# Performance work log

Hardware: AMD Instinct MI355X
Metric: run time of the kernel (lower is better)

The kernel has to match this reference:

```python
import jax, jax.numpy as jnp
from jax import lax
import numpy as np

N_HEADS, N_FEATURES, IMG_W, IMG_H, C_DOWN = 8, 64, 96, 96, 32


def setup_inputs() -> dict:
    key = jax.random.key(0)
    ks = jax.random.split(key, 16)
    d = {
        'X': jax.random.normal(ks[0], (N_FEATURES, IMG_W, IMG_H), jnp.float32),
        'WQ_task': jax.random.normal(ks[1], (N_HEADS, N_FEATURES, 1, 1), jnp.float32),
        'BQ_task': jax.random.normal(ks[2], (N_HEADS, N_FEATURES, 1, 1), jnp.float32),
        'WK_task': jax.random.normal(ks[3], (N_FEATURES, 1, 1), jnp.float32),
        'BK_task': jax.random.normal(ks[4], (N_FEATURES, 1, 1), jnp.float32),
        'WV_task': jax.random.normal(ks[5], (1, C_DOWN, 1, 1), jnp.float32),
        'BV_task': jax.random.normal(ks[6], (1, C_DOWN, 1, 1), jnp.float32),
        # learned parameters (loaded from disk in the original)
        'WQ_t_minus_1': jax.random.uniform(ks[7], (N_HEADS, N_FEATURES, 1, 1), jnp.float32),
        'WQ_x': jax.random.uniform(ks[8], (1, N_FEATURES, 1, 1), jnp.float32),
        'BQ': jax.random.uniform(ks[9], (N_HEADS, N_FEATURES, 1, 1), jnp.float32),
        'WK_x': jax.random.uniform(ks[10], (N_FEATURES, 1, 1), jnp.float32),
        'BK': jax.random.uniform(ks[11], (N_FEATURES, 1, 1), jnp.float32),
        'Vconv_w': jax.random.normal(ks[12], (C_DOWN, N_FEATURES, 3, 3), jnp.float32) * 0.05,
        'Vconv_b': jax.random.normal(ks[13], (C_DOWN,), jnp.float32) * 0.05,
        # recurrent state (zeros at t=0 in original; random here to exercise the path)
        'prev_Q': jax.random.normal(ks[14], (N_HEADS, N_FEATURES, IMG_W, IMG_H), jnp.float32),
    }
    return d


def reference(X, WQ_task, BQ_task, WK_task, BK_task, WV_task, BV_task,
              WQ_t_minus_1, WQ_x, BQ, WK_x, BK, Vconv_w, Vconv_b, prev_Q):
    F, W, H = X.shape
    rx = X[None]  # (1, F, W, H)
    # Q: (A, F, W, H);  K: (F, W, H)
    Q = WQ_task * jax.nn.relu(WQ_t_minus_1 * prev_Q + WQ_x * rx + BQ) + BQ_task
    K = WK_task * jax.nn.relu(WK_x * X + BK) + BK_task
    # similarity[w,h,u,v] = sum_{a,f} Q[a,f,w,h] * K[f,u,v]
    #                     = sum_f (sum_a Q)[f,w,h] * K[f,u,v]  -> a (WH,F)@(F,WH) GEMM
    Qs = Q.sum(axis=0)  # (F, W, H)
    sim = jnp.einsum('fwh,fuv->whuv', Qs, K)  # (W, H, W, H)
    attn = jax.nn.softmax(sim.reshape(W, H, W * H), axis=-1)  # (W, H, WH)
    # V = task-modulated 3x3 conv of X
    Vc = lax.conv_general_dilated(rx, Vconv_w, window_strides=(1, 1), padding='SAME',
                                  dimension_numbers=('NCHW', 'OIHW', 'NCHW'))
    Vc = Vc + Vconv_b[None, :, None, None]
    V = (WV_task * Vc + BV_task)[0].reshape(C_DOWN, W * H)  # (C, WH)
    # out[c,w,h] = sum_k attn[w,h,k] * V[c,k]
    out = jnp.einsum('whk,ck->cwh', attn, V)  # (C, W, H)
    return out
```

## Files before the change

### kernel.cpp

```cpp
#include <hip/hip_runtime.h>

#define WH 9216
#define NF 64
#define NC 32
#define NH 8
#define IMGW 96
#define IMGH 96
#define PW 98
#define PPLANE 9604
#define L2E 1.4426950408889634f
#define DEFER 11.5f

typedef float f32x4 __attribute__((ext_vector_type(4)));
typedef short short8 __attribute__((ext_vector_type(8)));

__device__ inline short bf16_bits(float x) {
  __bf16 h = (__bf16)x;
  return __builtin_bit_cast(short, h);
}
__device__ inline float bf16_round(float x) { return (float)(__bf16)x; }

__global__ __launch_bounds__(256, 2) void prep_kernel(
    const float* __restrict__ X, const float* __restrict__ WQ_task,
    const float* __restrict__ BQ_task, const float* __restrict__ WK_task,
    const float* __restrict__ BK_task, const float* __restrict__ WQ_t1,
    const float* __restrict__ WQ_x, const float* __restrict__ BQ,
    const float* __restrict__ WK_x, const float* __restrict__ BK,
    const float* __restrict__ prevQ, const float* __restrict__ Wc,
    const float* __restrict__ WV_task,
    short* __restrict__ qfrag, short* __restrict__ kfrag,
    unsigned short* __restrict__ padXT, short8* __restrict__ wfrag)
{
  const int bid = blockIdx.x;
  const int t = threadIdx.x;
  if (bid < 576) {
    const int lane = t & 63;
    const int w2 = t >> 6;
    const int fh = w2 & 1, sub = w2 >> 1;
    const int h = lane >> 4;
    const int T = bid;
    const int wh = T * 16 + (lane & 15);
    const int f0 = fh * 32 + 8 * h + 4 * sub;

    float x[4];
    #pragma unroll
    for (int e = 0; e < 4; ++e) x[e] = X[(size_t)(f0 + e) * WH + wh];
    float pq[32];
    #pragma unroll
    for (int a = 0; a < NH; ++a)
      #pragma unroll
      for (int e = 0; e < 4; ++e)
        pq[a * 4 + e] = prevQ[(size_t)(a * 64 + f0 + e) * WH + wh];

    const float4 wkx = *(const float4*)&WK_x[f0];
    const float4 bk  = *(const float4*)&BK[f0];
    const float4 wkt = *(const float4*)&WK_task[f0];
    const float4 bkt = *(const float4*)&BK_task[f0];
    const float4 wqx = *(const float4*)&WQ_x[f0];

    float q[4], k[4], xq[4];
    k[0] = fmaf(wkt.x, fmaxf(fmaf(wkx.x, x[0], bk.x), 0.f), bkt.x);
    k[1] = fmaf(wkt.y, fmaxf(fmaf(wkx.y, x[1], bk.y), 0.f), bkt.y);
    k[2] = fmaf(wkt.z, fmaxf(fmaf(wkx.z, x[2], bk.z), 0.f), bkt.z);
    k[3] = fmaf(wkt.w, fmaxf(fmaf(wkx.w, x[3], bk.w), 0.f), bkt.w);
    xq[0] = wqx.x * x[0]; xq[1] = wqx.y * x[1];
    xq[2] = wqx.z * x[2]; xq[3] = wqx.w * x[3];
    q[0] = q[1] = q[2] = q[3] = 0.f;
    #pragma unroll
    for (int a = 0; a < NH; ++a) {
      const int af0 = a * 64 + f0;
      const float4 w1  = *(const float4*)&WQ_t1[af0];
      const float4 bq  = *(const float4*)&BQ[af0];
      const float4 wqt = *(const float4*)&WQ_task[af0];
      const float4 bqt = *(const float4*)&BQ_task[af0];
      q[0] = fmaf(wqt.x, fmaxf(fmaf(w1.x, pq[a * 4 + 0], xq[0] + bq.x), 0.f), q[0]) + bqt.x;
      q[1] = fmaf(wqt.y, fmaxf(fmaf(w1.y, pq[a * 4 + 1], xq[1] + bq.y), 0.f), q[1]) + bqt.y;
      q[2] = fmaf(wqt.z, fmaxf(fmaf(w1.z, pq[a * 4 + 2], xq[2] + bq.z), 0.f), q[2]) + bqt.z;
      q[3] = fmaf(wqt.w, fmaxf(fmaf(w1.w, pq[a * 4 + 3], xq[3] + bq.w), 0.f), q[3]) + bqt.w;
    }

    short4 qh, ql, kh, klo;
    {
      float qs0 = q[0] * L2E, qs1 = q[1] * L2E, qs2 = q[2] * L2E, qs3 = q[3] * L2E;
      qh.x = bf16_bits(qs0); ql.x = bf16_bits(qs0 - bf16_round(qs0));
      qh.y = bf16_bits(qs1); ql.y = bf16_bits(qs1 - bf16_round(qs1));
      qh.z = bf16_bits(qs2); ql.z = bf16_bits(qs2 - bf16_round(qs2));
      qh.w = bf16_bits(qs3); ql.w = bf16_bits(qs3 - bf16_round(qs3));
      kh.x = bf16_bits(k[0]); klo.x = bf16_bits(k[0] - bf16_round(k[0]));
      kh.y = bf16_bits(k[1]); klo.y = bf16_bits(k[1] - bf16_round(k[1]));
      kh.z = bf16_bits(k[2]); klo.z = bf16_bits(k[2] - bf16_round(k[2]));
      kh.w = bf16_bits(k[3]); klo.w = bf16_bits(k[3] - bf16_round(k[3]));
    }
    const size_t offh = ((size_t)(T * 4 + fh) * 64 + lane) * 8 + sub * 4;
    const size_t offl = ((size_t)(T * 4 + 2 + fh) * 64 + lane) * 8 + sub * 4;
    *(short4*)&qfrag[offh] = qh;
    *(short4*)&qfrag[offl] = ql;
    *(short4*)&kfrag[offh] = kh;
    *(short4*)&kfrag[offl] = klo;
  } else if (bid < 877) {
    const int idx = (bid - 576) * 256 + t;
    if (idx < 76832) {
      const int fi = idx / PPLANE;
      const int p = idx - fi * PPLANE;
      const int pw = p / PW;
      const int ph = p - pw * PW;
      short8 r;
      if (pw >= 1 && pw <= IMGW && ph >= 1 && ph <= IMGH) {
        const float* src = X + (size_t)fi * 8 * WH + (pw - 1) * IMGH + (ph - 1);
        #pragma unroll
        for (int e = 0; e < 8; ++e) r[e] = bf16_bits(src[(size_t)e * WH]);
      } else {
        #pragma unroll
        for (int e = 0; e < 8; ++e) r[e] = 0;
      }
      *(short8*)&padXT[(size_t)p * 64 + fi * 8] = r;
    }
  } else {
    #pragma unroll
    for (int j = 0; j < 9; ++j) {
      const int ridx = j * 256 + t;
      const int ct = ridx / 1152;
      const int rem = ridx - ct * 1152;
      const int cc = rem >> 6;
      const int lane = rem & 63;
      const int c = ct * 16 + (lane & 15);
      const int tap = cc >> 1;
      const int f0 = (cc & 1) * 32 + 8 * (lane >> 4);
      const float wv = WV_task[c];
      short8 r;
      #pragma unroll
      for (int e = 0; e < 8; ++e)
        r[e] = bf16_bits(wv * Wc[((size_t)c * NF + f0 + e) * 9 + tap]);
      wfrag[ridx] = r;
    }
  }
}

__global__ __launch_bounds__(256, 2) void vconv_kernel(
    const unsigned short* __restrict__ padXT, const short8* __restrict__ wfrag,
    const float* __restrict__ bc, const float* __restrict__ WV_task,
    const float* __restrict__ BV_task, short* __restrict__ vfrag)
{
  __shared__ float Vt[2][32][20];
  const int t = threadIdx.x;
  const int lane = t & 63, w = t >> 6;
  const int h = lane >> 4;
  const int ktile = blockIdx.x;
  const int half = w & 1, ct = w >> 1;
  const int key = ktile * 16 + (lane & 15);
  const int kw = key / IMGH, kh = key - kw * IMGH;

  f32x4 acc = {0.f, 0.f, 0.f, 0.f};
  #pragma unroll
  for (int i = 0; i < 9; ++i) {
    const int cc = half * 9 + i;
    const int tap = cc >> 1;
    const int di = tap / 3, dj = tap - di * 3;
    const int f0 = (cc & 1) * 32 + 8 * h;
    const int sp = (kw + di) * PW + (kh + dj);
    const short8 xf = *(const short8*)&padXT[(size_t)sp * 64 + f0];
    acc = __builtin_amdgcn_mfma_f32_16x16x32_bf16(wfrag[(size_t)(ct * 18 + cc) * 64 + lane],
                                                  xf, acc, 0, 0, 0);
  }
  #pragma unroll
  for (int reg = 0; reg < 4; ++reg)
    Vt[half][ct * 16 + 4 * h + reg][lane & 15] = acc[reg];
  __syncthreads();
  if (t < 128) {
    const int ct2 = t >> 6;
    const int c = ct2 * 16 + (lane & 15);
    const float bias = fmaf(WV_task[c], bc[c], BV_task[c]);
    short4 r;
    #pragma unroll
    for (int j = 0; j < 4; ++j) {
      const int kl = 4 * h + j;
      r[j] = bf16_bits(Vt[0][c][kl] + Vt[1][c][kl] + bias);
    }
    const int ch = ktile >> 1, eh = ktile & 1;
    *(short4*)&vfrag[(((size_t)ch * 2 + ct2) * 64 + lane) * 8 + eh * 4] = r;
  }
}

__global__ __launch_bounds__(256, 3) void flash_mfma(
    const short8* __restrict__ qfrag, const short8* __restrict__ kfrag,
    const short8* __restrict__ vfrag, float* __restrict__ part, int cps)
{
  const int t = threadIdx.x;
  const int lane = t & 63, wave = t >> 6;
  const int h = lane >> 4;
  const int qb = blockIdx.x;
  const int s = blockIdx.y;

  short8 qf[3][4];
  #pragma unroll
  for (int g = 0; g < 3; ++g)
    #pragma unroll
    for (int tm = 0; tm < 4; ++tm)
      qf[g][tm] = qfrag[((size_t)(qb * 3 + g) * 4 + tm) * 64 + lane];

  f32x4 acc[2][3];
  #pragma unroll
  for (int ct = 0; ct < 2; ++ct)
    #pragma unroll
    for (int g = 0; g < 3; ++g)
      acc[ct][g] = (f32x4){0.f, 0.f, 0.f, 0.f};
  float m[3] = {0.f, 0.f, 0.f};
  float l[3] = {0.f, 0.f, 0.f};

  const int cpw = cps >> 2;
  const int ch0 = s * cps + wave;
  #pragma unroll 2
  for (int it = 0; it < cpw; ++it) {
    const int ch = ch0 + it * 4;
    short8 kf[2][4];
    #pragma unroll
    for (int kt = 0; kt < 2; ++kt)
      #pragma unroll
      for (int tm = 0; tm < 4; ++tm)
        kf[kt][tm] = kfrag[((size_t)(2 * ch + kt) * 4 + tm) * 64 + lane];
    const short8 vf0 = vfrag[(size_t)(ch * 2 + 0) * 64 + lane];
    const short8 vf1 = vfrag[(size_t)(ch * 2 + 1) * 64 + lane];

    f32x4 st[3][2];
    __builtin_amdgcn_s_setprio(1);
    #pragma unroll
    for (int g = 0; g < 3; ++g) {
      const float nm = -m[g];
      f32x4 a0 = {nm, nm, nm, nm};
      f32x4 a1 = a0;
      a0 = __builtin_amdgcn_mfma_f32_16x16x32_bf16(kf[0][0], qf[g][0], a0, 0, 0, 0);
      a0 = __builtin_amdgcn_mfma_f32_16x16x32_bf16(kf[0][1], qf[g][1], a0, 0, 0, 0);
      a0 = __builtin_amdgcn_mfma_f32_16x16x32_bf16(kf[0][2], qf[g][0], a0, 0, 0, 0);
      a0 = __builtin_amdgcn_mfma_f32_16x16x32_bf16(kf[0][3], qf[g][1], a0, 0, 0, 0);
      a0 = __builtin_amdgcn_mfma_f32_16x16x32_bf16(kf[0][0], qf[g][2], a0, 0, 0, 0);
      a0 = __builtin_amdgcn_mfma_f32_16x16x32_bf16(kf[0][1], qf[g][3], a0, 0, 0, 0);
      a1 = __builtin_amdgcn_mfma_f32_16x16x32_bf16(kf[1][0], qf[g][0], a1, 0, 0, 0);
      a1 = __builtin_amdgcn_mfma_f32_16x16x32_bf16(kf[1][1], qf[g][1], a1, 0, 0, 0);
      a1 = __builtin_amdgcn_mfma_f32_16x16x32_bf16(kf[1][2], qf[g][0], a1, 0, 0, 0);
      a1 = __builtin_amdgcn_mfma_f32_16x16x32_bf16(kf[1][3], qf[g][1], a1, 0, 0, 0);
      a1 = __builtin_amdgcn_mfma_f32_16x16x32_bf16(kf[1][0], qf[g][2], a1, 0, 0, 0);
      a1 = __builtin_amdgcn_mfma_f32_16x16x32_bf16(kf[1][1], qf[g][3], a1, 0, 0, 0);
      st[g][0] = a0;
      st[g][1] = a1;
    }
    __builtin_amdgcn_s_setprio(0);

    short8 pb[3];
    #pragma unroll
    for (int g = 0; g < 3; ++g) {
      f32x4 st0 = st[g][0], st1 = st[g][1];
      const float loc = fmaxf(fmaxf(fmaxf(st0[0], st0[1]), fmaxf(st0[2], st0[3])),
                              fmaxf(fmaxf(st1[0], st1[1]), fmaxf(st1[2], st1[3])));
      if (__any(loc > DEFER)) {
        float tr = loc;
        tr = fmaxf(tr, __shfl_xor(tr, 16));
        tr = fmaxf(tr, __shfl_xor(tr, 32));
        const float d = fmaxf(tr, 0.f);
        const float r = exp2f(-d);
        l[g] *= r;
        acc[0][g] *= r;
        acc[1][g] *= r;
        m[g] += d;
        #pragma unroll
        for (int e = 0; e < 4; ++e) { st0[e] -= d; st1[e] -= d; }
      }
      float p0[4], p1[4];
      #pragma unroll
      for (int e = 0; e < 4; ++e) {
        p0[e] = exp2f(st0[e]);
        p1[e] = exp2f(st1[e]);
        pb[g][e] = bf16_bits(p0[e]);
        pb[g][4 + e] = bf16_bits(p1[e]);
      }
      l[g] += ((p0[0] + p0[1]) + (p0[2] + p0[3])) + ((p1[0] + p1[1]) + (p1[2] + p1[3]));
    }

    __builtin_amdgcn_s_setprio(1);
    #pragma unroll
    for (int g = 0; g < 3; ++g) {
      acc[0][g] = __builtin_amdgcn_mfma_f32_16x16x32_bf16(vf0, pb[g], acc[0][g], 0, 0, 0);
      acc[1][g] = __builtin_amdgcn_mfma_f32_16x16x32_bf16(vf1, pb[g], acc[1][g], 0, 0, 0);
    }
    __builtin_amdgcn_s_setprio(0);
  }

  const int u = s * 4 + wave;
  #pragma unroll
  for (int g = 0; g < 3; ++g) {
    float lf = l[g] + __shfl_xor(l[g], 16);
    lf += __shfl_xor(lf, 32);
    const int q = qb * 48 + g * 16 + (lane & 15);
    float* base = part + ((size_t)u * WH + q) * 36;
    *(f32x4*)(base + 0 + 4 * h) = acc[0][g];
    *(f32x4*)(base + 16 + 4 * h) = acc[1][g];
    if (h == 0) { base[32] = m[g]; base[33] = lf; }
  }
}

__global__ __launch_bounds__(256) void merge_kernel(
    const float* __restrict__ part, float* __restrict__ out, int units)
{
  const int t = threadIdx.x;
  const int cl = t & 31;
  const int wh = blockIdx.x * 8 + (t >> 5);
  float M = -1e30f, L = 0.f, A = 0.f;
  for (int u = 0; u < units; ++u) {
    const float* base = part + ((size_t)u * WH + wh) * 36;
    const float mu = base[32];
    const float lu = base[33];
    const float au = base[cl];
    if (mu > M) {
      const float sc = exp2f(M - mu);
      L = fmaf(L, sc, lu);
      A = fmaf(A, sc, au);
      M = mu;
    } else {
      const float e = exp2f(mu - M);
      L = fmaf(e, lu, L);
      A = fmaf(e, au, A);
    }
  }
  out[(size_t)cl * WH + wh] = A / L;
}

extern "C" void kernel_launch(void* const* d_in, const int* in_sizes, int n_in,
                              void* d_out, int out_size, void* d_ws, size_t ws_size,
                              hipStream_t stream)
{
  const float* X   = (const float*)d_in[0];
  const float* WQt = (const float*)d_in[1];
  const float* BQt = (const float*)d_in[2];
  const float* WKt = (const float*)d_in[3];
  const float* BKt = (const float*)d_in[4];
  const float* WVt = (const float*)d_in[5];
  const float* BVt = (const float*)d_in[6];
  const float* WQ1 = (const float*)d_in[7];
  const float* WQx = (const float*)d_in[8];
  const float* BQ  = (const float*)d_in[9];
  const float* WKx = (const float*)d_in[10];
  const float* BK  = (const float*)d_in[11];
  const float* Wc  = (const float*)d_in[12];
  const float* bc  = (const float*)d_in[13];
  const float* pQ  = (const float*)d_in[14];
  float* out = (float*)d_out;

  short8* qfrag = (short8*)d_ws;
  short8* kfrag = qfrag + (size_t)147456;
  short8* vfrag = kfrag + (size_t)147456;
  short8* wfrag = vfrag + (size_t)36864;
  unsigned short* padXT = (unsigned short*)(wfrag + 2304);
  float* part = (float*)((char*)padXT + (size_t)PPLANE * 64 * 2);
  const size_t base_bytes = ((size_t)147456 * 2 + 36864 + 2304) * 16 + (size_t)PPLANE * 64 * 2;

  int ksplit = 4;
  while (ksplit > 1 &&
         base_bytes + (size_t)(4 * ksplit) * WH * 36 * sizeof(float) > ws_size)
    ksplit >>= 1;
  const int cps = 288 / ksplit;
  const int units = 4 * ksplit;

  prep_kernel<<<dim3(878), 256, 0, stream>>>(X, WQt, BQt, WKt, BKt,
                                             WQ1, WQx, BQ, WKx, BK, pQ, Wc, WVt,
                                             (short*)qfrag, (short*)kfrag, padXT, wfrag);
  vconv_kernel<<<dim3(576), 256, 0, stream>>>(padXT, wfrag, bc, WVt, BVt, (short*)vfrag);
  flash_mfma<<<dim3(192, ksplit), 256, 0, stream>>>(qfrag, kfrag, vfrag, part, cps);
  merge_kernel<<<dim3(WH / 8), 256, 0, stream>>>(part, out, units);
}
```

Before: 81.08 us.

## Rebalance prep stages and shrink flash query tile to two groups per wave

The Q/K fragment computation moves out of the padding/weight-pack kernel and into the V-conv kernel, so the small pad+pack kernel runs first and the larger combined kernel does both the elementwise Q/K work and the conv. This balances per-kernel work and lets Q/K production overlap with conv blocks. The flash attention kernel now handles 32 queries per block instead of 48, giving 288 blocks per split with launch bounds raised to 4 blocks per SM. That improves grid fill and occupancy at the cost of more K/V fragment reloads per query.

```diff
diff --git a/kernel.cpp b/kernel.cpp
--- a/kernel.cpp
+++ b/kernel.cpp
@@ -20,85 +20,15 @@
 }
 __device__ inline float bf16_round(float x) { return (float)(__bf16)x; }
 
-__global__ __launch_bounds__(256, 2) void prep_kernel(
-    const float* __restrict__ X, const float* __restrict__ WQ_task,
-    const float* __restrict__ BQ_task, const float* __restrict__ WK_task,
-    const float* __restrict__ BK_task, const float* __restrict__ WQ_t1,
-    const float* __restrict__ WQ_x, const float* __restrict__ BQ,
-    const float* __restrict__ WK_x, const float* __restrict__ BK,
-    const float* __restrict__ prevQ, const float* __restrict__ Wc,
+__global__ __launch_bounds__(256, 2) void pad_wpack_kernel(
+    const float* __restrict__ X, const float* __restrict__ Wc,
     const float* __restrict__ WV_task,
-    short* __restrict__ qfrag, short* __restrict__ kfrag,
     unsigned short* __restrict__ padXT, short8* __restrict__ wfrag)
 {
   const int bid = blockIdx.x;
   const int t = threadIdx.x;
-  if (bid < 576) {
-    const int lane = t & 63;
-    const int w2 = t >> 6;
-    const int fh = w2 & 1, sub = w2 >> 1;
-    const int h = lane >> 4;
-    const int T = bid;
-    const int wh = T * 16 + (lane & 15);
-    const int f0 = fh * 32 + 8 * h + 4 * sub;
-
-    float x[4];
-    #pragma unroll
-    for (int e = 0; e < 4; ++e) x[e] = X[(size_t)(f0 + e) * WH + wh];
-    float pq[32];
-    #pragma unroll
-    for (int a = 0; a < NH; ++a)
-      #pragma unroll
-      for (int e = 0; e < 4; ++e)
-        pq[a * 4 + e] = prevQ[(size_t)(a * 64 + f0 + e) * WH + wh];
-
-    const float4 wkx = *(const float4*)&WK_x[f0];
-    const float4 bk  = *(const float4*)&BK[f0];
-    const float4 wkt = *(const float4*)&WK_task[f0];
-    const float4 bkt = *(const float4*)&BK_task[f0];
-    const float4 wqx = *(const float4*)&WQ_x[f0];
-
-    float q[4], k[4], xq[4];
-    k[0] = fmaf(wkt.x, fmaxf(fmaf(wkx.x, x[0], bk.x), 0.f), bkt.x);
-    k[1] = fmaf(wkt.y, fmaxf(fmaf(wkx.y, x[1], bk.y), 0.f), bkt.y);
-    k[2] = fmaf(wkt.z, fmaxf(fmaf(wkx.z, x[2], bk.z), 0.f), bkt.z);
-    k[3] = fmaf(wkt.w, fmaxf(fmaf(wkx.w, x[3], bk.w), 0.f), bkt.w);
-    xq[0] = wqx.x * x[0]; xq[1] = wqx.y * x[1];
-    xq[2] = wqx.z * x[2]; xq[3] = wqx.w * x[3];
-    q[0] = q[1] = q[2] = q[3] = 0.f;
-    #pragma unroll
-    for (int a = 0; a < NH; ++a) {
-      const int af0 = a * 64 + f0;
-      const float4 w1  = *(const float4*)&WQ_t1[af0];
-      const float4 bq  = *(const float4*)&BQ[af0];
-      const float4 wqt = *(const float4*)&WQ_task[af0];
-      const float4 bqt = *(const float4*)&BQ_task[af0];
-      q[0] = fmaf(wqt.x, fmaxf(fmaf(w1.x, pq[a * 4 + 0], xq[0] + bq.x), 0.f), q[0]) + bqt.x;
-      q[1] = fmaf(wqt.y, fmaxf(fmaf(w1.y, pq[a * 4 + 1], xq[1] + bq.y), 0.f), q[1]) + bqt.y;
-      q[2] = fmaf(wqt.z, fmaxf(fmaf(w1.z, pq[a * 4 + 2], xq[2] + bq.z), 0.f), q[2]) + bqt.z;
-      q[3] = fmaf(wqt.w, fmaxf(fmaf(w1.w, pq[a * 4 + 3], xq[3] + bq.w), 0.f), q[3]) + bqt.w;
-    }
-
-    short4 qh, ql, kh, klo;
-    {
-      float qs0 = q[0] * L2E, qs1 = q[1] * L2E, qs2 = q[2] * L2E, qs3 = q[3] * L2E;
-      qh.x = bf16_bits(qs0); ql.x = bf16_bits(qs0 - bf16_round(qs0));
-      qh.y = bf16_bits(qs1); ql.y = bf16_bits(qs1 - bf16_round(qs1));
-      qh.z = bf16_bits(qs2); ql.z = bf16_bits(qs2 - bf16_round(qs2));
-      qh.w = bf16_bits(qs3); ql.w = bf16_bits(qs3 - bf16_round(qs3));
-      kh.x = bf16_bits(k[0]); klo.x = bf16_bits(k[0] - bf16_round(k[0]));
-      kh.y = bf16_bits(k[1]); klo.y = bf16_bits(k[1] - bf16_round(k[1]));
-      kh.z = bf16_bits(k[2]); klo.z = bf16_bits(k[2] - bf16_round(k[2]));
-      kh.w = bf16_bits(k[3]); klo.w = bf16_bits(k[3] - bf16_round(k[3]));
-    }
-    const size_t offh = ((size_t)(T * 4 + fh) * 64 + lane) * 8 + sub * 4;
-    const size_t offl = ((size_t)(T * 4 + 2 + fh) * 64 + lane) * 8 + sub * 4;
-    *(short4*)&qfrag[offh] = qh;
-    *(short4*)&qfrag[offl] = ql;
-    *(short4*)&kfrag[offh] = kh;
-    *(short4*)&kfrag[offl] = klo;
-  } else if (bid < 877) {
-    const int idx = (bid - 576) * 256 + t;
+  if (bid < 301) {
+    const int idx = bid * 256 + t;
     if (idx < 76832) {
       const int fi = idx / PPLANE;
       const int p = idx - fi * PPLANE;
@@ -136,52 +66,126 @@
   }
 }
 
-__global__ __launch_bounds__(256, 2) void vconv_kernel(
+__global__ __launch_bounds__(256, 2) void qsk_vconv_kernel(
+    const float* __restrict__ X, const float* __restrict__ WQ_task,
+    const float* __restrict__ BQ_task, const float* __restrict__ WK_task,
+    const float* __restrict__ BK_task, const float* __restrict__ WQ_t1,
+    const float* __restrict__ WQ_x, const float* __restrict__ BQ,
+    const float* __restrict__ WK_x, const float* __restrict__ BK,
+    const float* __restrict__ prevQ,
     const unsigned short* __restrict__ padXT, const short8* __restrict__ wfrag,
     const float* __restrict__ bc, const float* __restrict__ WV_task,
-    const float* __restrict__ BV_task, short* __restrict__ vfrag)
+    const float* __restrict__ BV_task,
+    short* __restrict__ qfrag, short* __restrict__ kfrag,
+    short* __restrict__ vfrag)
 {
   __shared__ float Vt[2][32][20];
+  const int bid = blockIdx.x;
   const int t = threadIdx.x;
-  const int lane = t & 63, w = t >> 6;
+  const int lane = t & 63;
   const int h = lane >> 4;
-  const int ktile = blockIdx.x;
-  const int half = w & 1, ct = w >> 1;
-  const int key = ktile * 16 + (lane & 15);
-  const int kw = key / IMGH, kh = key - kw * IMGH;
-
-  f32x4 acc = {0.f, 0.f, 0.f, 0.f};
-  #pragma unroll
-  for (int i = 0; i < 9; ++i) {
-    const int cc = half * 9 + i;
-    const int tap = cc >> 1;
-    const int di = tap / 3, dj = tap - di * 3;
-    const int f0 = (cc & 1) * 32 + 8 * h;
-    const int sp = (kw + di) * PW + (kh + dj);
-    const short8 xf = *(const short8*)&padXT[(size_t)sp * 64 + f0];
-    acc = __builtin_amdgcn_mfma_f32_16x16x32_bf16(wfrag[(size_t)(ct * 18 + cc) * 64 + lane],
-                                                  xf, acc, 0, 0, 0);
-  }
-  #pragma unroll
-  for (int reg = 0; reg < 4; ++reg)
-    Vt[half][ct * 16 + 4 * h + reg][lane & 15] = acc[reg];
-  __syncthreads();
-  if (t < 128) {
-    const int ct2 = t >> 6;
-    const int c = ct2 * 16 + (lane & 15);
-    const float bias = fmaf(WV_task[c], bc[c], BV_task[c]);
-    short4 r;
-    #pragma unroll
-    for (int j = 0; j < 4; ++j) {
-      const int kl = 4 * h + j;
-      r[j] = bf16_bits(Vt[0][c][kl] + Vt[1][c][kl] + bias);
-    }
-    const int ch = ktile >> 1, eh = ktile & 1;
-    *(short4*)&vfrag[(((size_t)ch * 2 + ct2) * 64 + lane) * 8 + eh * 4] = r;
-  }
-}
-
-__global__ __launch_bounds__(256, 3) void flash_mfma(
+  if (bid < 576) {
+    const int w2 = t >> 6;
+    const int fh = w2 & 1, sub = w2 >> 1;
+    const int T = bid;
+    const int wh = T * 16 + (lane & 15);
+    const int f0 = fh * 32 + 8 * h + 4 * sub;
+
+    float x[4];
+    #pragma unroll
+    for (int e = 0; e < 4; ++e) x[e] = X[(size_t)(f0 + e) * WH + wh];
+    float pq[32];
+    #pragma unroll
+    for (int a = 0; a < NH; ++a)
+      #pragma unroll
+      for (int e = 0; e < 4; ++e)
+        pq[a * 4 + e] = prevQ[(size_t)(a * 64 + f0 + e) * WH + wh];
+
+    const float4 wkx = *(const float4*)&WK_x[f0];
+    const float4 bk  = *(const float4*)&BK[f0];
+    const float4 wkt = *(const float4*)&WK_task[f0];
+    const float4 bkt = *(const float4*)&BK_task[f0];
+    const float4 wqx = *(const float4*)&WQ_x[f0];
+
+    float q[4], k[4], xq[4];
+    k[0] = fmaf(wkt.x, fmaxf(fmaf(wkx.x, x[0], bk.x), 0.f), bkt.x);
+    k[1] = fmaf(wkt.y, fmaxf(fmaf(wkx.y, x[1], bk.y), 0.f), bkt.y);
+    k[2] = fmaf(wkt.z, fmaxf(fmaf(wkx.z, x[2], bk.z), 0.f), bkt.z);
+    k[3] = fmaf(wkt.w, fmaxf(fmaf(wkx.w, x[3], bk.w), 0.f), bkt.w);
+    xq[0] = wqx.x * x[0]; xq[1] = wqx.y * x[1];
+    xq[2] = wqx.z * x[2]; xq[3] = wqx.w * x[3];
+    q[0] = q[1] = q[2] = q[3] = 0.f;
+    #pragma unroll
+    for (int a = 0; a < NH; ++a) {
+      const int af0 = a * 64 + f0;
+      const float4 w1  = *(const float4*)&WQ_t1[af0];
+      const float4 bq  = *(const float4*)&BQ[af0];
+      const float4 wqt = *(const float4*)&WQ_task[af0];
+      const float4 bqt = *(const float4*)&BQ_task[af0];
+      q[0] = fmaf(wqt.x, fmaxf(fmaf(w1.x, pq[a * 4 + 0], xq[0] + bq.x), 0.f), q[0]) + bqt.x;
+      q[1] = fmaf(wqt.y, fmaxf(fmaf(w1.y, pq[a * 4 + 1], xq[1] + bq.y), 0.f), q[1]) + bqt.y;
+      q[2] = fmaf(wqt.z, fmaxf(fmaf(w1.z, pq[a * 4 + 2], xq[2] + bq.z), 0.f), q[2]) + bqt.z;
+      q[3] = fmaf(wqt.w, fmaxf(fmaf(w1.w, pq[a * 4 + 3], xq[3] + bq.w), 0.f), q[3]) + bqt.w;
+    }
+
+    short4 qh, ql, kh, klo;
+    {
+      float qs0 = q[0] * L2E, qs1 = q[1] * L2E, qs2 = q[2] * L2E, qs3 = q[3] * L2E;
+      qh.x = bf16_bits(qs0); ql.x = bf16_bits(qs0 - bf16_round(qs0));
+      qh.y = bf16_bits(qs1); ql.y = bf16_bits(qs1 - bf16_round(qs1));
+      qh.z = bf16_bits(qs2); ql.z = bf16_bits(qs2 - bf16_round(qs2));
+      qh.w = bf16_bits(qs3); ql.w = bf16_bits(qs3 - bf16_round(qs3));
+      kh.x = bf16_bits(k[0]); klo.x = bf16_bits(k[0] - bf16_round(k[0]));
+      kh.y = bf16_bits(k[1]); klo.y = bf16_bits(k[1] - bf16_round(k[1]));
+      kh.z = bf16_bits(k[2]); klo.z = bf16_bits(k[2] - bf16_round(k[2]));
+      kh.w = bf16_bits(k[3]); klo.w = bf16_bits(k[3] - bf16_round(k[3]));
+    }
+    const size_t offh = ((size_t)(T * 4 + fh) * 64 + lane) * 8 + sub * 4;
+    const size_t offl = ((size_t)(T * 4 + 2 + fh) * 64 + lane) * 8 + sub * 4;
+    *(short4*)&qfrag[offh] = qh;
+    *(short4*)&qfrag[offl] = ql;
+    *(short4*)&kfrag[offh] = kh;
+    *(short4*)&kfrag[offl] = klo;
+  } else {
+    const int ktile = bid - 576;
+    const int w = t >> 6;
+    const int half = w & 1, ct = w >> 1;
+    const int key = ktile * 16 + (lane & 15);
+    const int kw = key / IMGH, kh = key - kw * IMGH;
+
+    f32x4 acc = {0.f, 0.f, 0.f, 0.f};
+    #pragma unroll
+    for (int i = 0; i < 9; ++i) {
+      const int cc = half * 9 + i;
+      const int tap = cc >> 1;
+      const int di = tap / 3, dj = tap - di * 3;
+      const int f0 = (cc & 1) * 32 + 8 * h;
+      const int sp = (kw + di) * PW + (kh + dj);
+      const short8 xf = *(const short8*)&padXT[(size_t)sp * 64 + f0];
+      acc = __builtin_amdgcn_mfma_f32_16x16x32_bf16(wfrag[(size_t)(ct * 18 + cc) * 64 + lane],
+                                                    xf, acc, 0, 0, 0);
+    }
+    #pragma unroll
+    for (int reg = 0; reg < 4; ++reg)
+      Vt[half][ct * 16 + 4 * h + reg][lane & 15] = acc[reg];
+    __syncthreads();
+    if (t < 128) {
+      const int ct2 = t >> 6;
+      const int c = ct2 * 16 + (lane & 15);
+      const float bias = fmaf(WV_task[c], bc[c], BV_task[c]);
+      short4 r;
+      #pragma unroll
+      for (int j = 0; j < 4; ++j) {
+        const int kl = 4 * h + j;
+        r[j] = bf16_bits(Vt[0][c][kl] + Vt[1][c][kl] + bias);
+      }
+      const int chh = ktile >> 1, eh = ktile & 1;
+      *(short4*)&vfrag[(((size_t)chh * 2 + ct2) * 64 + lane) * 8 + eh * 4] = r;
+    }
+  }
+}
+
+__global__ __launch_bounds__(256, 4) void flash_mfma(
     const short8* __restrict__ qfrag, const short8* __restrict__ kfrag,
     const short8* __restrict__ vfrag, float* __restrict__ part, int cps)
 {
@@ -191,21 +195,21 @@
   const int qb = blockIdx.x;
   const int s = blockIdx.y;
 
-  short8 qf[3][4];
+  short8 qf[2][4];
   #pragma unroll
-  for (int g = 0; g < 3; ++g)
+  for (int g = 0; g < 2; ++g)
     #pragma unroll
     for (int tm = 0; tm < 4; ++tm)
-      qf[g][tm] = qfrag[((size_t)(qb * 3 + g) * 4 + tm) * 64 + lane];
-
-  f32x4 acc[2][3];
+      qf[g][tm] = qfrag[((size_t)(qb * 2 + g) * 4 + tm) * 64 + lane];
+
+  f32x4 acc[2][2];
   #pragma unroll
   for (int ct = 0; ct < 2; ++ct)
     #pragma unroll
-    for (int g = 0; g < 3; ++g)
+    for (int g = 0; g < 2; ++g)
       acc[ct][g] = (f32x4){0.f, 0.f, 0.f, 0.f};
-  float m[3] = {0.f, 0.f, 0.f};
-  float l[3] = {0.f, 0.f, 0.f};
+  float m[2] = {0.f, 0.f};
+  float l[2] = {0.f, 0.f};
 
   const int cpw = cps >> 2;
   const int ch0 = s * cps + wave;
@@ -221,10 +225,10 @@
     const short8 vf0 = vfrag[(size_t)(ch * 2 + 0) * 64 + lane];
     const short8 vf1 = vfrag[(size_t)(ch * 2 + 1) * 64 + lane];
 
-    f32x4 st[3][2];
+    f32x4 st[2][2];
     __builtin_amdgcn_s_setprio(1);
     #pragma unroll
-    for (int g = 0; g < 3; ++g) {
+    for (int g = 0; g < 2; ++g) {
       const float nm = -m[g];
       f32x4 a0 = {nm, nm, nm, nm};
       f32x4 a1 = a0;
@@ -245,9 +249,9 @@
     }
     __builtin_amdgcn_s_setprio(0);
 
-    short8 pb[3];
-    #pragma unroll
-    for (int g = 0; g < 3; ++g) {
+    short8 pb[2];
+    #pragma unroll
+    for (int g = 0; g < 2; ++g) {
       f32x4 st0 = st[g][0], st1 = st[g][1];
       const float loc = fmaxf(fmaxf(fmaxf(st0[0], st0[1]), fmaxf(st0[2], st0[3])),
                               fmaxf(fmaxf(st1[0], st1[1]), fmaxf(st1[2], st1[3])));
@@ -277,7 +281,7 @@
 
     __builtin_amdgcn_s_setprio(1);
     #pragma unroll
-    for (int g = 0; g < 3; ++g) {
+    for (int g = 0; g < 2; ++g) {
       acc[0][g] = __builtin_amdgcn_mfma_f32_16x16x32_bf16(vf0, pb[g], acc[0][g], 0, 0, 0);
       acc[1][g] = __builtin_amdgcn_mfma_f32_16x16x32_bf16(vf1, pb[g], acc[1][g], 0, 0, 0);
     }
@@ -286,10 +290,10 @@
 
   const int u = s * 4 + wave;
   #pragma unroll
-  for (int g = 0; g < 3; ++g) {
+  for (int g = 0; g < 2; ++g) {
     float lf = l[g] + __shfl_xor(l[g], 16);
     lf += __shfl_xor(lf, 32);
-    const int q = qb * 48 + g * 16 + (lane & 15);
+    const int q = qb * 32 + g * 16 + (lane & 15);
     float* base = part + ((size_t)u * WH + q) * 36;
     *(f32x4*)(base + 0 + 4 * h) = acc[0][g];
     *(f32x4*)(base + 16 + 4 * h) = acc[1][g];
@@ -359,10 +363,12 @@
   const int cps = 288 / ksplit;
   const int units = 4 * ksplit;
 
-  prep_kernel<<<dim3(878), 256, 0, stream>>>(X, WQt, BQt, WKt, BKt,
-                                             WQ1, WQx, BQ, WKx, BK, pQ, Wc, WVt,
-                                             (short*)qfrag, (short*)kfrag, padXT, wfrag);
-  vconv_kernel<<<dim3(576), 256, 0, stream>>>(padXT, wfrag, bc, WVt, BVt, (short*)vfrag);
-  flash_mfma<<<dim3(192, ksplit), 256, 0, stream>>>(qfrag, kfrag, vfrag, part, cps);
+  pad_wpack_kernel<<<dim3(302), 256, 0, stream>>>(X, Wc, WVt, padXT, wfrag);
+  qsk_vconv_kernel<<<dim3(1152), 256, 0, stream>>>(X, WQt, BQt, WKt, BKt,
+                                                   WQ1, WQx, BQ, WKx, BK, pQ,
+                                                   padXT, wfrag, bc, WVt, BVt,
+                                                   (short*)qfrag, (short*)kfrag,
+                                                   (short*)vfrag);
+  flash_mfma<<<dim3(288, ksplit), 256, 0, stream>>>(qfrag, kfrag, vfrag, part, cps);
   merge_kernel<<<dim3(WH / 8), 256, 0, stream>>>(part, out, units);
 }
```

After: 87.14 us. 1.07x slower.
